# Optimization experiments

Hardware: AMD Instinct MI355X
Metric: run time of the kernel (lower is better)

## Reference

```python
import jax, jax.numpy as jnp
import numpy as np

D_MODEL = 1024
N_HEADS = 16
D_K = D_MODEL // N_HEADS


def setup_inputs() -> dict:
    key = jax.random.key(0)
    ks = jax.random.split(key, 9)
    s = 1.0 / np.sqrt(D_MODEL)
    x = jax.random.normal(ks[0], (2, 2048, D_MODEL), dtype=jnp.float32)
    Wq = jax.random.normal(ks[1], (D_MODEL, D_MODEL), dtype=jnp.float32) * s
    bq = jnp.zeros((D_MODEL,), jnp.float32)
    Wk = jax.random.normal(ks[2], (D_MODEL, D_MODEL), dtype=jnp.float32) * s
    bk = jnp.zeros((D_MODEL,), jnp.float32)
    Wv = jax.random.normal(ks[3], (D_MODEL, D_MODEL), dtype=jnp.float32) * s
    bv = jnp.zeros((D_MODEL,), jnp.float32)
    Wo = jax.random.normal(ks[4], (D_MODEL, D_MODEL), dtype=jnp.float32) * s
    bo = jnp.zeros((D_MODEL,), jnp.float32)
    return {"x": x, "Wq": Wq, "bq": bq, "Wk": Wk, "bk": bk,
            "Wv": Wv, "bv": bv, "Wo": Wo, "bo": bo}


def reference(x, Wq, bq, Wk, bk, Wv, bv, Wo, bo):
    B, T, C = x.shape
    H, Dk = N_HEADS, D_K
    # QKV projections, reshape to [B, H, T, Dk]
    q = (x @ Wq + bq).reshape(B, T, H, Dk).transpose(0, 2, 1, 3)
    k = (x @ Wk + bk).reshape(B, T, H, Dk).transpose(0, 2, 1, 3)
    v = (x @ Wv + bv).reshape(B, T, H, Dk).transpose(0, 2, 1, 3)
    scale = 1.0 / np.sqrt(Dk).astype(np.float32)
    att = jnp.einsum('bhqd,bhkd->bhqk', q, k) * scale  # [B,H,T,T]
    causal = jnp.tril(jnp.ones((T, T), dtype=bool))
    att = jnp.where(causal, att, -jnp.inf)
    att = jax.nn.softmax(att, axis=-1)
    y = jnp.einsum('bhqk,bhkd->bhqd', att, v)  # [B,H,T,Dk]
    y = y.transpose(0, 2, 1, 3).reshape(B, T, C)
    return y @ Wo + bo
```

## Files before the change

### kernel.cpp

```cpp
#include <hip/hip_runtime.h>
#include <stdint.h>

#define D_MODEL 1024
#define N_HEADS 16
#define D_K     64
#define T_SEQ   2048
#define BATCH   2
#define M_TOT   (BATCH * T_SEQ)
#define QCH     128

typedef __attribute__((ext_vector_type(8))) short  short8;
typedef __attribute__((ext_vector_type(4))) float  f32x4;
typedef __attribute__((ext_vector_type(4))) unsigned short u16x4;

typedef __attribute__((address_space(1))) void gvoid;
typedef __attribute__((address_space(3))) void lvoid;

#define QSCALE 0.18033688011112042f

static __device__ __forceinline__ unsigned short f2bf(float f) {
    union { float f; unsigned u; } v; v.f = f;
    unsigned u = v.u;
    u += 0x7fffu + ((u >> 16) & 1u);
    return (unsigned short)(u >> 16);
}
static __device__ __forceinline__ float bf2f(unsigned short s) {
    union { unsigned u; float f; } v; v.u = ((unsigned)s) << 16;
    return v.f;
}
static __device__ __forceinline__ float fexp2(float x) {
    float r;
    asm("v_exp_f32 %0, %1" : "=v"(r) : "v"(x));
    return r;
}
static __device__ __forceinline__ unsigned cvt_pk_bf16(float lo, float hi) {
    unsigned r;
    asm("v_cvt_pk_bf16_f32 %0, %1, %2" : "=v"(r) : "v"(lo), "v"(hi));
    return r;
}

__global__ void cvt_all(const float* __restrict__ x, unsigned short* __restrict__ xo,
                        const float* w0, const float* w1, const float* w2, const float* w3,
                        unsigned short* o0, unsigned short* o1, unsigned short* o2, unsigned short* o3) {
    if (blockIdx.z == 0) {
        const int tid = threadIdx.y * 32 + threadIdx.x;
        const int bid = blockIdx.y * 32 + blockIdx.x;
        const float4* in4 = (const float4*)x;
        #pragma unroll
        for (int j = 0; j < 4; ++j) {
            int i = bid * 256 + tid + j * 262144;
            float4 v = in4[i];
            u16x4 o;
            o.x = f2bf(v.x); o.y = f2bf(v.y); o.z = f2bf(v.z); o.w = f2bf(v.w);
            *(u16x4*)&xo[(size_t)i * 4] = o;
        }
        return;
    }
    const float* w; unsigned short* o;
    switch (blockIdx.z - 1) {
        case 0: w = w0; o = o0; break;
        case 1: w = w1; o = o1; break;
        case 2: w = w2; o = o2; break;
        default: w = w3; o = o3; break;
    }
    __shared__ float tile[32][33];
    int n0 = blockIdx.x * 32, k0 = blockIdx.y * 32;
    int tx = threadIdx.x, ty = threadIdx.y;
    #pragma unroll
    for (int r = 0; r < 32; r += 8)
        tile[ty + r][tx] = w[(size_t)(k0 + ty + r) * D_MODEL + n0 + tx];
    __syncthreads();
    #pragma unroll
    for (int r = 0; r < 32; r += 8)
        o[(size_t)(n0 + ty + r) * D_MODEL + k0 + tx] = f2bf(tile[tx][ty + r]);
}

__global__ __launch_bounds__(256) void gemm_qkv(const unsigned short* __restrict__ A,
                                                const unsigned short* __restrict__ wq,
                                                const unsigned short* __restrict__ wk,
                                                const unsigned short* __restrict__ wv,
                                                const float* __restrict__ bq,
                                                const float* __restrict__ bk,
                                                const float* __restrict__ bv,
                                                unsigned short* __restrict__ qo,
                                                unsigned short* __restrict__ ko,
                                                unsigned short* __restrict__ vo) {
    const int z = blockIdx.z;
    const unsigned short* Bt = (z == 0) ? wq : (z == 1) ? wk : wv;
    const float* bias = (z == 0) ? bq : (z == 1) ? bk : bv;
    const float alpha = (z == 0) ? QSCALE : 1.0f;

    __shared__ unsigned short lA[128 * 32];
    __shared__ unsigned short lB[128 * 32];
    const int tid  = threadIdx.x;
    const int w    = tid >> 6, lane = tid & 63;
    const int tm   = blockIdx.y, tn = blockIdx.x;
    const int wm   = w & 1, wn = w >> 1;
    const int i16  = lane & 15, g4 = lane >> 4;
    f32x4 acc[4][4] = {};

    const int rA0 = tm * 128, rB0 = tn * 128;
    const int srow = lane >> 2;
    const int skc  = (lane & 3) * 8;

    for (int k0 = 0; k0 < D_MODEL; k0 += 32) {
        #pragma unroll
        for (int is = 0; is < 2; ++is) {
            int c   = is * 4 + w;
            int row = c * 16 + srow;
            __builtin_amdgcn_global_load_lds(
                (gvoid*)(A + (size_t)(rA0 + row) * D_MODEL + k0 + skc),
                (lvoid*)&lA[c * 512], 16, 0, 0);
            __builtin_amdgcn_global_load_lds(
                (gvoid*)(Bt + (size_t)(rB0 + row) * D_MODEL + k0 + skc),
                (lvoid*)&lB[c * 512], 16, 0, 0);
        }
        __syncthreads();
        short8 af[4], bfr[4];
        #pragma unroll
        for (int mi = 0; mi < 4; ++mi)
            af[mi] = *(const short8*)&lA[(wm * 64 + mi * 16 + i16) * 32 + g4 * 8];
        #pragma unroll
        for (int ni = 0; ni < 4; ++ni)
            bfr[ni] = *(const short8*)&lB[(wn * 64 + ni * 16 + i16) * 32 + g4 * 8];
        #pragma unroll
        for (int mi = 0; mi < 4; ++mi)
            #pragma unroll
            for (int ni = 0; ni < 4; ++ni)
                acc[mi][ni] = __builtin_amdgcn_mfma_f32_16x16x32_bf16(af[mi], bfr[ni], acc[mi][ni], 0, 0, 0);
        __syncthreads();
    }

    #pragma unroll
    for (int mi = 0; mi < 4; ++mi)
        #pragma unroll
        for (int ni = 0; ni < 4; ++ni) {
            int col = tn * 128 + wn * 64 + ni * 16 + i16;
            float bv2 = bias[col];
            #pragma unroll
            for (int r = 0; r < 4; ++r) {
                int row = tm * 128 + wm * 64 + mi * 16 + g4 * 4 + r;
                float val = (acc[mi][ni][r] + bv2) * alpha;
                int b = row >> 11, t = row & (T_SEQ - 1);
                int h = col >> 6,  d = col & (D_K - 1);
                unsigned short bfv = f2bf(val);
                if (z == 2)
                    vo[(((size_t)(b * N_HEADS + h)) * D_K + d) * T_SEQ + t] = bfv;
                else if (z == 1)
                    ko[(((size_t)(b * N_HEADS + h)) * T_SEQ + t) * D_K + d] = bfv;
                else
                    qo[(((size_t)(b * N_HEADS + h)) * T_SEQ + t) * D_K + d] = bfv;
            }
        }
}

__global__ __launch_bounds__(256) void gemm_out(const unsigned short* __restrict__ A,
                                                const unsigned short* __restrict__ Bt,
                                                const float* __restrict__ bias,
                                                float* __restrict__ Cout) {
    __shared__ unsigned short lA[128 * 32];
    __shared__ unsigned short lB[64 * 32];
    const int tid  = threadIdx.x;
    const int w    = tid >> 6, lane = tid & 63;
    const int tm   = blockIdx.y, tn = blockIdx.x;
    const int wm   = w & 1, wn = w >> 1;
    const int i16  = lane & 15, g4 = lane >> 4;
    f32x4 acc[4][2] = {};

    const int rA0 = tm * 128, rB0 = tn * 64;
    const int srow = lane >> 2;
    const int skc  = (lane & 3) * 8;

    for (int k0 = 0; k0 < D_MODEL; k0 += 32) {
        #pragma unroll
        for (int is = 0; is < 2; ++is) {
            int c   = is * 4 + w;
            int row = c * 16 + srow;
            __builtin_amdgcn_global_load_lds(
                (gvoid*)(A + (size_t)(rA0 + row) * D_MODEL + k0 + skc),
                (lvoid*)&lA[c * 512], 16, 0, 0);
        }
        {
            int row = w * 16 + srow;
            __builtin_amdgcn_global_load_lds(
                (gvoid*)(Bt + (size_t)(rB0 + row) * D_MODEL + k0 + skc),
                (lvoid*)&lB[w * 512], 16, 0, 0);
        }
        __syncthreads();
        short8 af[4], bfr[2];
        #pragma unroll
        for (int mi = 0; mi < 4; ++mi)
            af[mi] = *(const short8*)&lA[(wm * 64 + mi * 16 + i16) * 32 + g4 * 8];
        #pragma unroll
        for (int ni = 0; ni < 2; ++ni)
            bfr[ni] = *(const short8*)&lB[(wn * 32 + ni * 16 + i16) * 32 + g4 * 8];
        #pragma unroll
        for (int mi = 0; mi < 4; ++mi)
            #pragma unroll
            for (int ni = 0; ni < 2; ++ni)
                acc[mi][ni] = __builtin_amdgcn_mfma_f32_16x16x32_bf16(af[mi], bfr[ni], acc[mi][ni], 0, 0, 0);
        __syncthreads();
    }

    #pragma unroll
    for (int mi = 0; mi < 4; ++mi)
        #pragma unroll
        for (int ni = 0; ni < 2; ++ni) {
            int col = tn * 64 + wn * 32 + ni * 16 + i16;
            float bv2 = bias[col];
            #pragma unroll
            for (int r = 0; r < 4; ++r) {
                int row = tm * 128 + wm * 64 + mi * 16 + g4 * 4 + r;
                Cout[(size_t)row * D_MODEL + col] = acc[mi][ni][r] + bv2;
            }
        }
}

__global__ __launch_bounds__(256, 3) void flash7(const unsigned short* __restrict__ q,
                                                 const unsigned short* __restrict__ k,
                                                 const unsigned short* __restrict__ vt,
                                                 unsigned short* __restrict__ op01,
                                                 unsigned short* __restrict__ op2,
                                                 float* __restrict__ lws) {
    __shared__ unsigned short lK[2][64 * 64];
    __shared__ unsigned short lV[2][64 * 64];
    __shared__ unsigned short lP[4][2][16 * 64];
    const int tid  = threadIdx.x;
    const int w    = tid >> 6, lane = tid & 63;
    const int i16  = lane & 15, g4 = lane >> 4;
    const int l8   = lane & 7,  g8 = lane >> 3;
    const int nb   = blockIdx.x;
    const int p    = nb & 7;
    const int s    = (nb >> 3) % 3;
    const int bh   = nb / 24;

    const unsigned short* kp = k  + (size_t)bh * T_SEQ * D_K;
    const unsigned short* vp = vt + (size_t)bh * D_K * T_SEQ;
    const int swz  = (i16 & 7) << 3;
    const int csrc = (l8 ^ g8) << 3;

    const int b = bh >> 4, hh = bh & 15;
    unsigned short* op = (s == 2) ? op2 : op01 + (size_t)s * ((size_t)M_TOT * D_MODEL);

    auto stage = [&](int buf, int kv0s) {
        #pragma unroll
        for (int i = 0; i < 2; ++i) {
            const int cidx = w * 2 + i;
            const int row  = cidx * 8 + g8;
            __builtin_amdgcn_global_load_lds(
                (gvoid*)(kp + (size_t)(kv0s + row) * D_K + csrc),
                (lvoid*)&lK[buf][cidx * 512], 16, 0, 0);
            __builtin_amdgcn_global_load_lds(
                (gvoid*)(vp + (size_t)row * T_SEQ + kv0s + csrc),
                (lvoid*)&lV[buf][cidx * 512], 16, 0, 0);
        }
    };

    #pragma unroll 1
    for (int ci = 0; ci < 2; ++ci) {
        const int c   = ci ? p : (15 - p);
        const int q0w = c * QCH + w * 32;
        const int cnt = (2 * c + 1 >= s) ? (2 * c + 1 - s) / 3 + 1 : 0;

        const unsigned short* qp = q + ((size_t)bh * T_SEQ + q0w) * D_K;
        short8 qf[2][2];
        #pragma unroll
        for (int qt = 0; qt < 2; ++qt)
            #pragma unroll
            for (int ks = 0; ks < 2; ++ks)
                qf[qt][ks] = *(const short8*)&qp[(qt * 16 + i16) * D_K + ks * 32 + g4 * 8];

        f32x4 o[2][4] = {};
        float l[2] = {0.f, 0.f};

        if (cnt > 0) stage(0, s * 64);
        __syncthreads();

        for (int it = 0; it < cnt; ++it) {
            const int cur = it & 1;
            const int kv0 = (s + 3 * it) * 64;
            if (it + 1 < cnt) stage(cur ^ 1, kv0 + 192);

            if (kv0 <= q0w + 31) {
                const bool act0 = (kv0 <= q0w + 15);
                const unsigned short* Kc = &lK[cur][0];
                const unsigned short* Vc = &lV[cur][0];

                f32x4 sA[4][2] = {};
                __builtin_amdgcn_s_setprio(1);
                #pragma unroll
                for (int ks = 0; ks < 2; ++ks)
                    #pragma unroll
                    for (int kt = 0; kt < 4; ++kt) {
                        short8 ka = *(const short8*)&Kc[(kt * 16 + i16) * 64 + ((ks * 32 + g4 * 8) ^ swz)];
                        if (act0)
                            sA[kt][0] = __builtin_amdgcn_mfma_f32_16x16x32_bf16(ka, qf[0][ks], sA[kt][0], 0, 0, 0);
                        sA[kt][1] = __builtin_amdgcn_mfma_f32_16x16x32_bf16(ka, qf[1][ks], sA[kt][1], 0, 0, 0);
                    }
                __builtin_amdgcn_s_setprio(0);

                #pragma unroll
                for (int qt = 0; qt < 2; ++qt) {
                    if (qt == 0 && !act0) continue;
                    const int qrow = q0w + qt * 16 + i16;
                    const bool diag = (kv0 + 63 > q0w + qt * 16);
                    float ps = 0.f;
                    unsigned pk[8];
                    #pragma unroll
                    for (int kt = 0; kt < 4; ++kt) {
                        f32x4 sc = sA[kt][qt];
                        if (diag) {
                            #pragma unroll
                            for (int r = 0; r < 4; ++r)
                                if (kv0 + kt * 16 + g4 * 4 + r > qrow) sc[r] = -3e38f;
                        }
                        float p0 = fexp2(sc[0]), p1 = fexp2(sc[1]);
                        float p2 = fexp2(sc[2]), p3 = fexp2(sc[3]);
                        ps += (p0 + p1) + (p2 + p3);
                        pk[kt * 2]     = cvt_pk_bf16(p0, p1);
                        pk[kt * 2 + 1] = cvt_pk_bf16(p2, p3);
                    }
                    l[qt] += ps;
                    unsigned short* Pw = &lP[w][qt][0];
                    #pragma unroll
                    for (int kt = 0; kt < 4; ++kt) {
                        uint2 v2; v2.x = pk[kt * 2]; v2.y = pk[kt * 2 + 1];
                        *(uint2*)&Pw[i16 * 64 + ((kt * 16 + g4 * 4) ^ swz)] = v2;
                    }
                }

                __builtin_amdgcn_s_setprio(1);
                #pragma unroll
                for (int qt = 0; qt < 2; ++qt) {
                    if (qt == 0 && !act0) continue;
                    const unsigned short* Pw = &lP[w][qt][0];
                    short8 pB0 = *(const short8*)&Pw[i16 * 64 + (( 0 + g4 * 8) ^ swz)];
                    short8 pB1 = *(const short8*)&Pw[i16 * 64 + ((32 + g4 * 8) ^ swz)];
                    #pragma unroll
                    for (int dt = 0; dt < 4; ++dt) {
                        short8 va0 = *(const short8*)&Vc[(dt * 16 + i16) * 64 + (( 0 + g4 * 8) ^ swz)];
                        short8 va1 = *(const short8*)&Vc[(dt * 16 + i16) * 64 + ((32 + g4 * 8) ^ swz)];
                        o[qt][dt] = __builtin_amdgcn_mfma_f32_16x16x32_bf16(va0, pB0, o[qt][dt], 0, 0, 0);
                        o[qt][dt] = __builtin_amdgcn_mfma_f32_16x16x32_bf16(va1, pB1, o[qt][dt], 0, 0, 0);
                    }
                }
                __builtin_amdgcn_s_setprio(0);
            }
            __syncthreads();
        }

        #pragma unroll
        for (int qt = 0; qt < 2; ++qt) {
            float lt = l[qt] + __shfl_xor(l[qt], 16);
            lt += __shfl_xor(lt, 32);
            const int trow = q0w + qt * 16 + i16;
            if (g4 == 0)
                lws[((size_t)s * 32 + bh) * T_SEQ + trow] = lt;
            #pragma unroll
            for (int dt = 0; dt < 4; ++dt) {
                u16x4 ov;
                ov.x = f2bf(o[qt][dt][0]);
                ov.y = f2bf(o[qt][dt][1]);
                ov.z = f2bf(o[qt][dt][2]);
                ov.w = f2bf(o[qt][dt][3]);
                *(u16x4*)&op[((size_t)(b * T_SEQ) + trow) * D_MODEL + hh * D_K + dt * 16 + g4 * 4] = ov;
            }
        }
        __syncthreads();
    }
}

__global__ __launch_bounds__(256) void merge3(const unsigned short* __restrict__ op01,
                                              const unsigned short* __restrict__ op2,
                                              const float* __restrict__ lws,
                                              unsigned short* __restrict__ y) {
    const int idx = blockIdx.x * 256 + threadIdx.x;
    const int gl  = idx * 8;
    const int row = gl >> 10;
    const int col = gl & 1023;
    const int b = row >> 11, t = row & (T_SEQ - 1), h = col >> 6;
    const int bh = b * 16 + h;
    const float l0 = lws[((size_t)bh) * T_SEQ + t];
    const float l1 = lws[((size_t)(32 + bh)) * T_SEQ + t];
    const float l2 = lws[((size_t)(64 + bh)) * T_SEQ + t];
    const float inv = 1.0f / (l0 + l1 + l2);
    short8 a0 = *(const short8*)&op01[gl];
    short8 a1 = *(const short8*)&op01[(size_t)M_TOT * D_MODEL + gl];
    short8 a2 = *(const short8*)&op2[gl];
    short8 r;
    #pragma unroll
    for (int j = 0; j < 8; ++j) {
        float f = bf2f((unsigned short)a0[j]) + bf2f((unsigned short)a1[j]) + bf2f((unsigned short)a2[j]);
        r[j] = (short)f2bf(f * inv);
    }
    *(short8*)&y[gl] = r;
}

extern "C" void kernel_launch(void* const* d_in, const int* in_sizes, int n_in,
                              void* d_out, int out_size, void* d_ws, size_t ws_size,
                              hipStream_t stream) {
    const float* x  = (const float*)d_in[0];
    const float* Wq = (const float*)d_in[1];
    const float* bq = (const float*)d_in[2];
    const float* Wk = (const float*)d_in[3];
    const float* bk = (const float*)d_in[4];
    const float* Wv = (const float*)d_in[5];
    const float* bv = (const float*)d_in[6];
    const float* Wo = (const float*)d_in[7];
    const float* bo = (const float*)d_in[8];

    uint8_t* ws = (uint8_t*)d_ws;
    const size_t MB = (size_t)1 << 20;
    unsigned short* xb  = (unsigned short*)(ws);
    unsigned short* wqt = (unsigned short*)(ws + 8  * MB);
    unsigned short* wkt = (unsigned short*)(ws + 10 * MB);
    unsigned short* wvt = (unsigned short*)(ws + 12 * MB);
    unsigned short* wot = (unsigned short*)(ws + 14 * MB);
    unsigned short* qb  = (unsigned short*)(ws + 16 * MB);
    unsigned short* kb  = (unsigned short*)(ws + 24 * MB);
    unsigned short* vtb = (unsigned short*)(ws + 32 * MB);
    float* lws = (float*)(ws + 8 * MB);

    cvt_all<<<dim3(32, 32, 5), dim3(32, 8), 0, stream>>>(x, xb, Wq, Wk, Wv, Wo, wqt, wkt, wvt, wot);

    gemm_qkv<<<dim3(8, 32, 3), 256, 0, stream>>>(xb, wqt, wkt, wvt, bq, bk, bv, qb, kb, vtb);

    flash7<<<768, 256, 0, stream>>>(qb, kb, vtb, (unsigned short*)d_out, xb, lws);
    merge3<<<2048, 256, 0, stream>>>((const unsigned short*)d_out, xb, lws, qb);

    gemm_out<<<dim3(16, 32), 256, 0, stream>>>(qb, wot, bo, (float*)d_out);
}
```

Baseline: 116.1 us.

## Triple-buffer QKV GEMM LDS tiles with async global-to-LDS prefetch

Replaces the single-buffered load/sync/compute loop in the QKV projection GEMM with a three-stage LDS ring. Tiles for step t+2 are issued via global_load_lds before computing step t, with explicit vmcnt waits and barriers. The aim is to hide global memory latency behind MFMA work and drop one barrier per iteration. It triples LDS use for the tiles, which may lower occupancy, and it depends on correct manual vmcnt accounting.

```diff
diff --git a/kernel.cpp b/kernel.cpp
--- a/kernel.cpp
+++ b/kernel.cpp
@@ -90,8 +90,8 @@
     const float* bias = (z == 0) ? bq : (z == 1) ? bk : bv;
     const float alpha = (z == 0) ? QSCALE : 1.0f;
 
-    __shared__ unsigned short lA[128 * 32];
-    __shared__ unsigned short lB[128 * 32];
+    __shared__ unsigned short lA[3][128 * 32];
+    __shared__ unsigned short lB[3][128 * 32];
     const int tid  = threadIdx.x;
     const int w    = tid >> 6, lane = tid & 63;
     const int tm   = blockIdx.y, tn = blockIdx.x;
@@ -103,32 +103,49 @@
     const int srow = lane >> 2;
     const int skc  = (lane & 3) * 8;
 
-    for (int k0 = 0; k0 < D_MODEL; k0 += 32) {
+    auto stage = [&](int buf, int k0) {
         #pragma unroll
         for (int is = 0; is < 2; ++is) {
             int c   = is * 4 + w;
             int row = c * 16 + srow;
             __builtin_amdgcn_global_load_lds(
                 (gvoid*)(A + (size_t)(rA0 + row) * D_MODEL + k0 + skc),
-                (lvoid*)&lA[c * 512], 16, 0, 0);
+                (lvoid*)&lA[buf][c * 512], 16, 0, 0);
             __builtin_amdgcn_global_load_lds(
                 (gvoid*)(Bt + (size_t)(rB0 + row) * D_MODEL + k0 + skc),
-                (lvoid*)&lB[c * 512], 16, 0, 0);
-        }
-        __syncthreads();
+                (lvoid*)&lB[buf][c * 512], 16, 0, 0);
+        }
+    };
+
+    stage(0, 0);
+    stage(1, 32);
+    asm volatile("s_waitcnt vmcnt(4)" ::: "memory");
+    __builtin_amdgcn_s_barrier();
+    __builtin_amdgcn_sched_barrier(0);
+
+    for (int t = 0; t < 32; ++t) {
+        const bool pre = (t + 2 < 32);
+        if (pre) stage((t + 2) % 3, (t + 2) * 32);
+
+        const unsigned short* cA = &lA[t % 3][0];
+        const unsigned short* cB = &lB[t % 3][0];
         short8 af[4], bfr[4];
         #pragma unroll
         for (int mi = 0; mi < 4; ++mi)
-            af[mi] = *(const short8*)&lA[(wm * 64 + mi * 16 + i16) * 32 + g4 * 8];
+            af[mi] = *(const short8*)&cA[(wm * 64 + mi * 16 + i16) * 32 + g4 * 8];
         #pragma unroll
         for (int ni = 0; ni < 4; ++ni)
-            bfr[ni] = *(const short8*)&lB[(wn * 64 + ni * 16 + i16) * 32 + g4 * 8];
+            bfr[ni] = *(const short8*)&cB[(wn * 64 + ni * 16 + i16) * 32 + g4 * 8];
         #pragma unroll
         for (int mi = 0; mi < 4; ++mi)
             #pragma unroll
             for (int ni = 0; ni < 4; ++ni)
                 acc[mi][ni] = __builtin_amdgcn_mfma_f32_16x16x32_bf16(af[mi], bfr[ni], acc[mi][ni], 0, 0, 0);
-        __syncthreads();
+
+        if (pre) asm volatile("s_waitcnt vmcnt(4)" ::: "memory");
+        else     asm volatile("s_waitcnt vmcnt(0)" ::: "memory");
+        __builtin_amdgcn_s_barrier();
+        __builtin_amdgcn_sched_barrier(0);
     }
 
     #pragma unroll
```

New measurement: 117.6 us. Within noise of the previous version (+1.3%).
